# Performance work log

Measured on AMD Instinct MI355X. Metric: run time of the kernel, lower is better.

## Reference

```python
import jax, jax.numpy as jnp
from jax import lax
import numpy as np

WINDOW_SIZES = (1, 2, 3)


def _proj(x, w1, b1, w2, b2):
    # gated projection: sigmoid(Linear1) * tanh(Linear2)
    return jax.nn.sigmoid(x @ w1.T + b1) * jnp.tanh(x @ w2.T + b2)


def setup_inputs() -> dict:
    key = jax.random.key(0)
    ks = jax.random.split(key, 16)
    V, E, D = 50000, 1024, 1024
    N, La, Lq = 64, 512, 64
    s = 0.02  # weight scale to keep sigmoid/tanh unsaturated
    return {
        "data_q": jax.random.randint(ks[0], (Lq,), 0, V),
        "data_as": jax.random.randint(ks[1], (N, La), 0, V),
        "emb": jax.random.normal(ks[2], (V, E), jnp.float32),
        "w1": jax.random.normal(ks[3], (D, E), jnp.float32) * s,
        "b1": jnp.zeros((D,), jnp.float32),
        "w2": jax.random.normal(ks[4], (D, E), jnp.float32) * s,
        "b2": jnp.zeros((D,), jnp.float32),
        "cw1": jax.random.normal(ks[5], (D, D, 1), jnp.float32) * s,
        "cb1": jnp.zeros((D,), jnp.float32),
        "cw2": jax.random.normal(ks[6], (D, D, 2), jnp.float32) * s,
        "cb2": jnp.zeros((D,), jnp.float32),
        "cw3": jax.random.normal(ks[7], (D, D, 3), jnp.float32) * s,
        "cb3": jnp.zeros((D,), jnp.float32),
        "lin_w": jax.random.normal(ks[8], (D, 3 * D), jnp.float32) * s,
        "lin_b": jnp.zeros((D,), jnp.float32),
        "soft_w": jax.random.normal(ks[9], (1, D), jnp.float32) * s,
        "soft_b": jnp.zeros((1,), jnp.float32),
    }


def reference(data_q, data_as, emb, w1, b1, w2, b2,
              cw1, cb1, cw2, cb2, cw3, cb3, lin_w, lin_b, soft_w, soft_b):
    N, La = data_as.shape
    a_tok = data_as.reshape(-1)                     # [T] concatenated answers
    emb_a = emb[a_tok]                              # [T, E]
    emb_q = emb[data_q]                             # [Lq, E]
    pa = _proj(emb_a, w1, b1, w2, b2)               # [T, D]
    pq = _proj(emb_q, w1, b1, w2, b2)               # [Lq, D]

    # attention: M_r = q @ a^T ; alpha = softmax over question positions
    M = pq @ pa.T                                   # [Lq, T]
    alpha = jax.nn.softmax(M.T, axis=1)             # [T, Lq]
    Y = alpha @ pq                                  # [T, D]
    sim = pa * Y                                    # elementwise compare (mul)

    starts = jnp.arange(N) * La
    x = sim.T[None]                                 # [1, D, T]
    pools = []
    for w, cw, cb in zip(WINDOW_SIZES, (cw1, cw2, cw3), (cb1, cb2, cb3)):
        conv = lax.conv_general_dilated(
            x, cw, (1,), 'VALID',
            dimension_numbers=('NCW', 'OIW', 'NCW'))[0].T + cb  # [T-w+1, D]
        conv = jax.nn.relu(conv)
        # DMax: per-answer max over rows [start_k, start_k + La - w + 1)
        idx = starts[:, None] + jnp.arange(La - w + 1)[None, :]  # [N, La-w+1]
        pools.append(conv[idx].max(axis=1))          # [N, D]

    cat = jnp.concatenate(pools, axis=1)            # [N, 3D]
    h = jnp.tanh(cat @ lin_w.T + lin_b)             # [N, D]
    logits = (h @ soft_w.T + soft_b).reshape(-1)    # [N]
    return jax.nn.log_softmax(logits)
```

## Files before the change

kernel.cpp:

```cpp
#include <hip/hip_runtime.h>

#define DEV __device__ __forceinline__

typedef __bf16 bf16x8 __attribute__((ext_vector_type(8)));
typedef float f32x4 __attribute__((ext_vector_type(4)));
typedef unsigned short u16;
typedef u16 u16x4 __attribute__((ext_vector_type(4)));

constexpr int T_ANS = 32768;
constexpr int LQ    = 64;
constexpr int M_ALL = T_ANS + LQ;
constexpr int M_PAD = 32896;
constexpr int DIM   = 1024;

DEV u16 f2bf(float x) {
  unsigned u = __float_as_uint(x);
  return (u16)((u + 0x7FFFu + ((u >> 16) & 1u)) >> 16);
}
DEV float bf2f(u16 s) { return __uint_as_float(((unsigned)s) << 16); }

DEV void gl2lds16(const void* g, void* l) {
  __builtin_amdgcn_global_load_lds(
      (const __attribute__((address_space(1))) unsigned int*)g,
      (__attribute__((address_space(3))) unsigned int*)l, 16, 0, 0);
}


__global__ void cast4(const float* __restrict__ src, u16* __restrict__ dst, int n4) {
  int i = blockIdx.x * 256 + threadIdx.x;
  if (i < n4) {
    float4 v = ((const float4*)src)[i];
    u16x4 o = { f2bf(v.x), f2bf(v.y), f2bf(v.z), f2bf(v.w) };
    ((u16x4*)dst)[i] = o;
  }
}

template<int W>
__global__ void cast_conv_w(const float* __restrict__ src, u16* __restrict__ dst) {
  int i = blockIdx.x * 256 + threadIdx.x;
  if (i < 1024 * 1024) {
#pragma unroll
    for (int k = 0; k < W; ++k)
      dst[(size_t)k * (1024 * 1024) + i] = f2bf(src[(size_t)i * W + k]);
  }
}

__global__ void gather_cast(const int* __restrict__ dq, const int* __restrict__ das,
                            const float* __restrict__ emb, u16* __restrict__ X) {
  const int row = blockIdx.x;
  const int c   = threadIdx.x;
  size_t dsto = (size_t)row * DIM + c * 4;
  if (row >= M_ALL) {
    u16x4 z = {0, 0, 0, 0};
    *(u16x4*)(X + dsto) = z;
    return;
  }
  const int tok = (row < T_ANS) ? das[row] : dq[row - T_ANS];
  float4 v = ((const float4*)(emb + (size_t)tok * DIM))[c];
  u16x4 o = { f2bf(v.x), f2bf(v.y), f2bf(v.z), f2bf(v.w) };
  *(u16x4*)(X + dsto) = o;
}

__global__ void transpose_pq(const u16* __restrict__ pa, u16* __restrict__ pqT) {
  int i = blockIdx.x * 256 + threadIdx.x;
  int e = i >> 6, q = i & 63;
  pqT[i] = pa[(size_t)(T_ANS + q) * DIM + e];
}

__global__ void zero_pad_sim(u16* __restrict__ sim) {
  int i = blockIdx.x * 256 + threadIdx.x;
  if (i < 2 * DIM) sim[(size_t)T_ANS * DIM + i] = 0;
}

__global__ void cast_cat(const float* __restrict__ cat, u16* __restrict__ catb) {
  int i = blockIdx.x * 256 + threadIdx.x;
  if (i < 128 * 3072) {
    int row = i / 3072;
    catb[i] = (row < 64) ? f2bf(cat[i]) : (u16)0;
  }
}


__global__ __launch_bounds__(512, 2)
void proj_dual(const u16* __restrict__ X, const u16* __restrict__ B1,
               const u16* __restrict__ B2, const float* __restrict__ b1,
               const float* __restrict__ b2, u16* __restrict__ pa) {
  __shared__ alignas(16) u16 sA[128 * 32];
  __shared__ alignas(16) u16 sB1[128 * 32];
  __shared__ alignas(16) u16 sB2[128 * 32];
  const int tid = threadIdx.x, lane = tid & 63;
  const int tm = blockIdx.x * 128, tn = blockIdx.y * 128;
  const int wid = tid >> 6;
  const int wm = (wid >> 1) * 32, wn = (wid & 1) * 64;
  f32x4 acc1[2][4] = {}, acc2[2][4] = {};
  for (int k0 = 0; k0 < 1024; k0 += 32) {
    {
      const int f = tid * 16;
      const int r = f >> 6, cb = f & 63;
      gl2lds16((const char*)X  + (size_t)(tm + r) * 2048 + k0 * 2 + cb, (char*)sA  + f);
      gl2lds16((const char*)B1 + (size_t)(tn + r) * 2048 + k0 * 2 + cb, (char*)sB1 + f);
      gl2lds16((const char*)B2 + (size_t)(tn + r) * 2048 + k0 * 2 + cb, (char*)sB2 + f);
    }
    __syncthreads();
    const int lr = lane & 15, lk = (lane >> 4) * 8;
    bf16x8 af[2], bv1[4], bv2[4];
#pragma unroll
    for (int i = 0; i < 2; ++i)
      af[i]  = *(const bf16x8*)(sA  + (wm + i * 16 + lr) * 32 + lk);
#pragma unroll
    for (int i = 0; i < 4; ++i) {
      bv1[i] = *(const bf16x8*)(sB1 + (wn + i * 16 + lr) * 32 + lk);
      bv2[i] = *(const bf16x8*)(sB2 + (wn + i * 16 + lr) * 32 + lk);
    }
#pragma unroll
    for (int mi = 0; mi < 2; ++mi)
#pragma unroll
      for (int ni = 0; ni < 4; ++ni) {
        acc1[mi][ni] = __builtin_amdgcn_mfma_f32_16x16x32_bf16(af[mi], bv1[ni], acc1[mi][ni], 0, 0, 0);
        acc2[mi][ni] = __builtin_amdgcn_mfma_f32_16x16x32_bf16(af[mi], bv2[ni], acc2[mi][ni], 0, 0, 0);
      }
    __syncthreads();
  }
  const int lr = lane & 15, lg = (lane >> 4) * 4;
#pragma unroll
  for (int ni = 0; ni < 4; ++ni) {
    const int col = tn + wn + ni * 16 + lr;
    const float b1v = b1[col], b2v = b2[col];
#pragma unroll
    for (int mi = 0; mi < 2; ++mi)
#pragma unroll
      for (int r = 0; r < 4; ++r) {
        const int row = tm + wm + mi * 16 + lg + r;
        const float x1 = acc1[mi][ni][r] + b1v;
        const float x2 = acc2[mi][ni][r] + b2v;
        const float sg = 1.f / (1.f + __expf(-x1));
        const float th = 2.f / (1.f + __expf(-2.f * x2)) - 1.f;
        pa[(size_t)row * DIM + col] = f2bf(sg * th);
      }
  }
}


__global__ __launch_bounds__(256, 2)
void attn_s(const u16* __restrict__ pa, float* __restrict__ Spart) {
  __shared__ alignas(16) u16 sA[128 * 32];
  __shared__ alignas(16) u16 sB[64 * 32];
  const int tid = threadIdx.x, lane = tid & 63;
  const int tm = blockIdx.x * 128;
  const int kbase = blockIdx.y * 256;
  const int wid = tid >> 6;
  const int wm = (wid >> 1) * 64, wn = (wid & 1) * 32;
  const u16* pq = pa + (size_t)T_ANS * DIM;
  f32x4 acc[4][2] = {};
  for (int k0 = kbase; k0 < kbase + 256; k0 += 32) {
#pragma unroll
    for (int j = 0; j < 2; ++j) {
      const int f = tid * 16 + j * 4096;
      const int r = f >> 6, cb = f & 63;
      gl2lds16((const char*)pa + (size_t)(tm + r) * 2048 + k0 * 2 + cb, (char*)sA + f);
    }
    {
      const int f = tid * 16;
      const int r = f >> 6, cb = f & 63;
      gl2lds16((const char*)pq + (size_t)r * 2048 + k0 * 2 + cb, (char*)sB + f);
    }
    __syncthreads();
    const int lr = lane & 15, lk = (lane >> 4) * 8;
    bf16x8 af[4], bfr[2];
#pragma unroll
    for (int i = 0; i < 4; ++i)
      af[i] = *(const bf16x8*)(sA + (wm + i * 16 + lr) * 32 + lk);
#pragma unroll
    for (int i = 0; i < 2; ++i)
      bfr[i] = *(const bf16x8*)(sB + (wn + i * 16 + lr) * 32 + lk);
#pragma unroll
    for (int mi = 0; mi < 4; ++mi)
#pragma unroll
      for (int ni = 0; ni < 2; ++ni)
        acc[mi][ni] = __builtin_amdgcn_mfma_f32_16x16x32_bf16(af[mi], bfr[ni], acc[mi][ni], 0, 0, 0);
    __syncthreads();
  }
  const int lr = lane & 15, lg = (lane >> 4) * 4;
  float* Sp = Spart + (size_t)blockIdx.y * (T_ANS * 64);
#pragma unroll
  for (int mi = 0; mi < 4; ++mi)
#pragma unroll
    for (int ni = 0; ni < 2; ++ni)
#pragma unroll
      for (int r = 0; r < 4; ++r) {
        const int row = tm + wm + mi * 16 + lg + r;
        const int col = wn + ni * 16 + lr;
        Sp[(size_t)row * 64 + col] = acc[mi][ni][r];
      }
}

__global__ void softmax64(const float* __restrict__ Spart, u16* __restrict__ alpha) {
  const int row = blockIdx.x * 4 + (threadIdx.x >> 6);
  const int lane = threadIdx.x & 63;
  const size_t o = (size_t)row * 64 + lane;
  float v = Spart[o] + Spart[(size_t)1 * T_ANS * 64 + o]
          + Spart[(size_t)2 * T_ANS * 64 + o] + Spart[(size_t)3 * T_ANS * 64 + o];
  float m = v;
#pragma unroll
  for (int o2 = 32; o2 > 0; o2 >>= 1) m = fmaxf(m, __shfl_xor(m, o2));
  const float e = __expf(v - m);
  float s = e;
#pragma unroll
  for (int o2 = 32; o2 > 0; o2 >>= 1) s += __shfl_xor(s, o2);
  alpha[(size_t)row * 64 + lane] = f2bf(e / s);
}


__global__ __launch_bounds__(256, 2)
void attn_y_sim(const u16* __restrict__ alpha, const u16* __restrict__ pqT,
                const u16* __restrict__ pa, u16* __restrict__ sim) {
  __shared__ alignas(16) u16 sA[128 * 32];
  __shared__ alignas(16) u16 sB[128 * 32];
  const int tid = threadIdx.x, lane = tid & 63;
  const int tm = blockIdx.x * 128, tn = blockIdx.y * 128;
  const int wid = tid >> 6;
  const int wm = (wid >> 1) * 64, wn = (wid & 1) * 64;
  f32x4 acc[4][4] = {};
  for (int k0 = 0; k0 < 64; k0 += 32) {
#pragma unroll
    for (int j = 0; j < 2; ++j) {
      const int f = tid * 16 + j * 4096;
      const int r = f >> 6, cb = f & 63;
      gl2lds16((const char*)alpha + (size_t)(tm + r) * 128 + k0 * 2 + cb, (char*)sA + f);
      gl2lds16((const char*)pqT   + (size_t)(tn + r) * 128 + k0 * 2 + cb, (char*)sB + f);
    }
    __syncthreads();
    const int lr = lane & 15, lk = (lane >> 4) * 8;
    bf16x8 af[4], bfr[4];
#pragma unroll
    for (int i = 0; i < 4; ++i) {
      af[i]  = *(const bf16x8*)(sA + (wm + i * 16 + lr) * 32 + lk);
      bfr[i] = *(const bf16x8*)(sB + (wn + i * 16 + lr) * 32 + lk);
    }
#pragma unroll
    for (int mi = 0; mi < 4; ++mi)
#pragma unroll
      for (int ni = 0; ni < 4; ++ni)
        acc[mi][ni] = __builtin_amdgcn_mfma_f32_16x16x32_bf16(af[mi], bfr[ni], acc[mi][ni], 0, 0, 0);
    __syncthreads();
  }
  const int lr = lane & 15, lg = (lane >> 4) * 4;
#pragma unroll
  for (int ni = 0; ni < 4; ++ni) {
    const int col = tn + wn + ni * 16 + lr;
#pragma unroll
    for (int mi = 0; mi < 4; ++mi)
#pragma unroll
      for (int r = 0; r < 4; ++r) {
        const int row = tm + wm + mi * 16 + lg + r;
        const size_t o = (size_t)row * DIM + col;
        sim[o] = f2bf(bf2f(pa[o]) * acc[mi][ni][r]);
      }
  }
}


template<int W>
__global__ __launch_bounds__(256, 2)
void conv_pool(const u16* __restrict__ sim, const u16* __restrict__ Bw,
               const float* __restrict__ cb, float* __restrict__ cat) {
  __shared__ alignas(16) u16 sA[(128 + W) * 32];
  __shared__ alignas(16) u16 sB[W][128 * 32];
  const int tid = threadIdx.x, lane = tid & 63;
  const int tm = blockIdx.x * 128, tn = blockIdx.y * 128;
  const int wid = tid >> 6;
  const int wm = (wid >> 1) * 64, wn = (wid & 1) * 64;
  f32x4 acc[4][4] = {};
  for (int k0 = 0; k0 < 1024; k0 += 32) {
#pragma unroll
    for (int j = 0; j < 2; ++j) {
      const int f = tid * 16 + j * 4096;
      const int r = f >> 6, cbo = f & 63;
      gl2lds16((const char*)sim + (size_t)(tm + r) * 2048 + k0 * 2 + cbo, (char*)sA + f);
#pragma unroll
      for (int k = 0; k < W; ++k)
        gl2lds16((const char*)Bw + (size_t)k * 2097152 + (size_t)(tn + r) * 2048 + k0 * 2 + cbo,
                 (char*)&sB[k][0] + f);
    }
    if (W > 1 && tid < (W - 1) * 4) {
      const int f = 8192 + tid * 16;
      const int r = f >> 6, cbo = f & 63;
      gl2lds16((const char*)sim + (size_t)(tm + r) * 2048 + k0 * 2 + cbo, (char*)sA + f);
    }
    __syncthreads();
    const int lr = lane & 15, lk = (lane >> 4) * 8;
#pragma unroll
    for (int k = 0; k < W; ++k) {
      bf16x8 af[4], bfr[4];
#pragma unroll
      for (int i = 0; i < 4; ++i) {
        af[i]  = *(const bf16x8*)(sA + (wm + i * 16 + lr + k) * 32 + lk);
        bfr[i] = *(const bf16x8*)(&sB[k][0] + (wn + i * 16 + lr) * 32 + lk);
      }
#pragma unroll
      for (int mi = 0; mi < 4; ++mi)
#pragma unroll
        for (int ni = 0; ni < 4; ++ni)
          acc[mi][ni] = __builtin_amdgcn_mfma_f32_16x16x32_bf16(af[mi], bfr[ni], acc[mi][ni], 0, 0, 0);
    }
    __syncthreads();
  }
  const int lr = lane & 15, lg = (lane >> 4) * 4;
  const int n = tm >> 9;
#pragma unroll
  for (int ni = 0; ni < 4; ++ni) {
    const int col = tn + wn + ni * 16 + lr;
    const float cbv = cb[col];
    float vmax = 0.f;
#pragma unroll
    for (int mi = 0; mi < 4; ++mi)
#pragma unroll
      for (int r = 0; r < 4; ++r) {
        const int t = tm + wm + mi * 16 + lg + r;
        float v = fmaxf(acc[mi][ni][r] + cbv, 0.f);
        if ((t & 511) > 512 - W) v = 0.f;
        vmax = fmaxf(vmax, v);
      }
    vmax = fmaxf(vmax, __shfl_xor(vmax, 16));
    vmax = fmaxf(vmax, __shfl_xor(vmax, 32));
    if (lane < 16)
      atomicMax((int*)&cat[(size_t)n * 3072 + (W - 1) * 1024 + col], __float_as_int(vmax));
  }
}


__global__ __launch_bounds__(256, 2)
void final_h(const u16* __restrict__ catb, const u16* __restrict__ linb,
             const float* __restrict__ lin_b, float* __restrict__ h) {
  __shared__ alignas(16) u16 sA[128 * 32];
  __shared__ alignas(16) u16 sB[128 * 32];
  const int tid = threadIdx.x, lane = tid & 63;
  const int tn = blockIdx.y * 128;
  const int wid = tid >> 6;
  const int wm = (wid >> 1) * 64, wn = (wid & 1) * 64;
  f32x4 acc[4][4] = {};
  for (int k0 = 0; k0 < 3072; k0 += 32) {
#pragma unroll
    for (int j = 0; j < 2; ++j) {
      const int f = tid * 16 + j * 4096;
      const int r = f >> 6, cb = f & 63;
      gl2lds16((const char*)catb + (size_t)r * 6144 + k0 * 2 + cb, (char*)sA + f);
      gl2lds16((const char*)linb + (size_t)(tn + r) * 6144 + k0 * 2 + cb, (char*)sB + f);
    }
    __syncthreads();
    const int lr = lane & 15, lk = (lane >> 4) * 8;
    bf16x8 af[4], bfr[4];
#pragma unroll
    for (int i = 0; i < 4; ++i) {
      af[i]  = *(const bf16x8*)(sA + (wm + i * 16 + lr) * 32 + lk);
      bfr[i] = *(const bf16x8*)(sB + (wn + i * 16 + lr) * 32 + lk);
    }
#pragma unroll
    for (int mi = 0; mi < 4; ++mi)
#pragma unroll
      for (int ni = 0; ni < 4; ++ni)
        acc[mi][ni] = __builtin_amdgcn_mfma_f32_16x16x32_bf16(af[mi], bfr[ni], acc[mi][ni], 0, 0, 0);
    __syncthreads();
  }
  const int lr = lane & 15, lg = (lane >> 4) * 4;
#pragma unroll
  for (int ni = 0; ni < 4; ++ni) {
    const int col = tn + wn + ni * 16 + lr;
    const float bv = lin_b[col];
#pragma unroll
    for (int mi = 0; mi < 4; ++mi)
#pragma unroll
      for (int r = 0; r < 4; ++r) {
        const int row = wm + mi * 16 + lg + r;
        if (row < 64) {
          const float x = acc[mi][ni][r] + bv;
          h[(size_t)row * DIM + col] = 2.f / (1.f + __expf(-2.f * x)) - 1.f;
        }
      }
  }
}

__global__ void final_logits(const float* __restrict__ h, const float* __restrict__ soft_w,
                             const float* __restrict__ soft_b, float* __restrict__ out) {
  __shared__ float part[256];
  const int t = threadIdx.x;
  const int n = t >> 2, q = t & 3;
  float s = 0.f;
  for (int j = q * 256; j < q * 256 + 256; ++j) s += h[(size_t)n * DIM + j] * soft_w[j];
  part[t] = s;
  __syncthreads();
  if (t < 64) {
    float logit = part[t * 4] + part[t * 4 + 1] + part[t * 4 + 2] + part[t * 4 + 3] + soft_b[0];
    float m = logit;
#pragma unroll
    for (int o = 32; o > 0; o >>= 1) m = fmaxf(m, __shfl_xor(m, o));
    float e = __expf(logit - m);
    float ssum = e;
#pragma unroll
    for (int o = 32; o > 0; o >>= 1) ssum += __shfl_xor(ssum, o);
    out[t] = (logit - m) - logf(ssum);
  }
}


extern "C" void kernel_launch(void* const* d_in, const int* in_sizes, int n_in,
                              void* d_out, int out_size, void* d_ws, size_t ws_size,
                              hipStream_t stream) {
  const int*   data_q  = (const int*)d_in[0];
  const int*   data_as = (const int*)d_in[1];
  const float* emb     = (const float*)d_in[2];
  const float* w1      = (const float*)d_in[3];
  const float* b1      = (const float*)d_in[4];
  const float* w2      = (const float*)d_in[5];
  const float* b2      = (const float*)d_in[6];
  const float* cw1     = (const float*)d_in[7];
  const float* cb1     = (const float*)d_in[8];
  const float* cw2     = (const float*)d_in[9];
  const float* cb2     = (const float*)d_in[10];
  const float* cw3     = (const float*)d_in[11];
  const float* cb3     = (const float*)d_in[12];
  const float* lin_w   = (const float*)d_in[13];
  const float* lin_b   = (const float*)d_in[14];
  const float* soft_w  = (const float*)d_in[15];
  const float* soft_b  = (const float*)d_in[16];
  float* out = (float*)d_out;

  u16* X     = (u16*)d_ws;
  u16* pa    = X    + (size_t)M_PAD * DIM;
  u16* w1b   = pa   + (size_t)M_PAD * DIM;
  u16* w2b   = w1b  + 1024 * 1024;
  u16* cwb   = w2b  + 1024 * 1024;
  u16* linb  = cwb  + (size_t)6 * 1024 * 1024;
  u16* pqT   = linb + (size_t)3 * 1024 * 1024;
  u16* alpha = pqT  + 64 * 1024;
  float* Sold= (float*)(alpha + (size_t)T_ANS * 64);
  float* cat = Sold + (size_t)T_ANS * 64;
  u16* catb  = (u16*)(cat + 64 * 3072);
  float* h   = (float*)(catb + 128 * 3072);
  u16* simb  = X;
  float* Spart = (float*)X;

  hipMemsetAsync(cat, 0, 64 * 3072 * sizeof(float), stream);

  cast4<<<1024, 256, 0, stream>>>(w1, w1b, 1024 * 1024 / 4);
  cast4<<<1024, 256, 0, stream>>>(w2, w2b, 1024 * 1024 / 4);
  cast4<<<3072, 256, 0, stream>>>(lin_w, linb, 3072 * 1024 / 4);
  cast_conv_w<1><<<4096, 256, 0, stream>>>(cw1, cwb);
  cast_conv_w<2><<<4096, 256, 0, stream>>>(cw2, cwb + (size_t)1 * 1024 * 1024);
  cast_conv_w<3><<<4096, 256, 0, stream>>>(cw3, cwb + (size_t)3 * 1024 * 1024);

  gather_cast<<<M_PAD, 256, 0, stream>>>(data_q, data_as, emb, X);

  proj_dual<<<dim3(M_PAD / 128, 8), 512, 0, stream>>>(X, w1b, w2b, b1, b2, pa);
  transpose_pq<<<256, 256, 0, stream>>>(pa, pqT);

  attn_s<<<dim3(T_ANS / 128, 4), 256, 0, stream>>>(pa, Spart);
  softmax64<<<T_ANS / 4, 256, 0, stream>>>(Spart, alpha);
  attn_y_sim<<<dim3(T_ANS / 128, 8), 256, 0, stream>>>(alpha, pqT, pa, simb);
  zero_pad_sim<<<8, 256, 0, stream>>>(simb);

  conv_pool<1><<<dim3(T_ANS / 128, 8), 256, 0, stream>>>(simb, cwb, cb1, cat);
  conv_pool<2><<<dim3(T_ANS / 128, 8), 256, 0, stream>>>(simb, cwb + (size_t)1 * 1024 * 1024, cb2, cat);
  conv_pool<3><<<dim3(T_ANS / 128, 8), 256, 0, stream>>>(simb, cwb + (size_t)3 * 1024 * 1024, cb3, cat);

  cast_cat<<<1536, 256, 0, stream>>>(cat, catb);
  final_h<<<dim3(1, 8), 256, 0, stream>>>(catb, linb, lin_b, h);
  final_logits<<<1, 256, 0, stream>>>(h, soft_w, soft_b, out);
}
```

Baseline: 865.1 us.

## Replace projection and conv GEMMs with 256x256 double-buffered swizzled-LDS pipeline

Introduces a shared GEMM pipeline macro using 256x256 tiles, 128KB dynamic LDS, an XOR-swizzled layout, and double-buffered async global-to-LDS staging interleaved with MFMA phases under s_setprio and explicit waitcnt control. The projection now uses a single packed W12 weight that interleaves w1 and w2 in 16-row groups, so one GEMM yields both gates per tile. The conv kernels treat the W-tap convolution as a K=1024*W GEMM, with the shifted A rows addressed directly through the A pointer. M_PAD grows to fit 256-row tiles. The intent is to cut LDS traffic and exposed memory latency and raise MFMA utilisation, at the cost of one block per CU and fewer blocks in the grid.

Measured after the change: 930.7 us. 7.6% more time.

```diff
diff --git a/kernel.cpp b/kernel.cpp
--- a/kernel.cpp
+++ b/kernel.cpp
@@ -10,7 +10,7 @@
 constexpr int T_ANS = 32768;
 constexpr int LQ    = 64;
 constexpr int M_ALL = T_ANS + LQ;
-constexpr int M_PAD = 32896;
+constexpr int M_PAD = 33024;
 constexpr int DIM   = 1024;
 
 DEV u16 f2bf(float x) {
@@ -24,6 +24,93 @@
       (const __attribute__((address_space(1))) unsigned int*)g,
       (__attribute__((address_space(3))) unsigned int*)l, 16, 0, 0);
 }
+
+#define MF(A, B, C) __builtin_amdgcn_mfma_f32_16x16x32_bf16(A, B, C, 0, 0, 0)
+
+
+DEV void stageC(const char* gk, char* ldsT, int row0, int tid) {
+  const int f = tid << 4;
+  const int r = row0 + (f >> 7);
+  const int cb = ((f >> 4) & 7) ^ (r & 7);
+  gl2lds16(gk + (size_t)r * 2048 + (cb << 4), ldsT + (row0 << 7) + f);
+}
+
+DEV bf16x8 LF(const char* ldsT, int row, int cbyte) {
+  return *(const bf16x8*)(ldsT + (row << 7) + (cbyte ^ ((row & 7) << 4)));
+}
+
+#define PH(Q, LA, LB, STAGES, VMW)                                                     \
+  {                                                                                    \
+    bf16x8 a00 = LF(LA, wm + (2*(Q))*16 + lr, hi16);                                   \
+    bf16x8 a01 = LF(LA, wm + (2*(Q))*16 + lr, 64 + hi16);                              \
+    bf16x8 a10 = LF(LA, wm + (2*(Q)+1)*16 + lr, hi16);                                 \
+    bf16x8 a11 = LF(LA, wm + (2*(Q)+1)*16 + lr, 64 + hi16);                            \
+    bf16x8 b00 = LF(LB, wn +  0 + lr, hi16), b01 = LF(LB, wn +  0 + lr, 64 + hi16);    \
+    bf16x8 b10 = LF(LB, wn + 16 + lr, hi16), b11 = LF(LB, wn + 16 + lr, 64 + hi16);    \
+    bf16x8 b20 = LF(LB, wn + 32 + lr, hi16), b21 = LF(LB, wn + 32 + lr, 64 + hi16);    \
+    bf16x8 b30 = LF(LB, wn + 48 + lr, hi16), b31 = LF(LB, wn + 48 + lr, 64 + hi16);    \
+    STAGES                                                                             \
+    __builtin_amdgcn_s_barrier();                                                      \
+    asm volatile("s_waitcnt lgkmcnt(0)" ::: "memory");                                 \
+    __builtin_amdgcn_sched_barrier(0);                                                 \
+    __builtin_amdgcn_s_setprio(1);                                                     \
+    acc[2*(Q)][0] = MF(a00, b00, acc[2*(Q)][0]); acc[2*(Q)][0] = MF(a01, b01, acc[2*(Q)][0]); \
+    acc[2*(Q)][1] = MF(a00, b10, acc[2*(Q)][1]); acc[2*(Q)][1] = MF(a01, b11, acc[2*(Q)][1]); \
+    acc[2*(Q)][2] = MF(a00, b20, acc[2*(Q)][2]); acc[2*(Q)][2] = MF(a01, b21, acc[2*(Q)][2]); \
+    acc[2*(Q)][3] = MF(a00, b30, acc[2*(Q)][3]); acc[2*(Q)][3] = MF(a01, b31, acc[2*(Q)][3]); \
+    acc[2*(Q)+1][0] = MF(a10, b00, acc[2*(Q)+1][0]); acc[2*(Q)+1][0] = MF(a11, b01, acc[2*(Q)+1][0]); \
+    acc[2*(Q)+1][1] = MF(a10, b10, acc[2*(Q)+1][1]); acc[2*(Q)+1][1] = MF(a11, b11, acc[2*(Q)+1][1]); \
+    acc[2*(Q)+1][2] = MF(a10, b20, acc[2*(Q)+1][2]); acc[2*(Q)+1][2] = MF(a11, b21, acc[2*(Q)+1][2]); \
+    acc[2*(Q)+1][3] = MF(a10, b30, acc[2*(Q)+1][3]); acc[2*(Q)+1][3] = MF(a11, b31, acc[2*(Q)+1][3]); \
+    __builtin_amdgcn_s_setprio(0);                                                     \
+    VMW                                                                                \
+    __builtin_amdgcn_s_barrier();                                                      \
+  }
+
+#define VM2 asm volatile("s_waitcnt vmcnt(2)" ::: "memory"); __builtin_amdgcn_sched_barrier(0);
+#define VM0 asm volatile("s_waitcnt vmcnt(0)" ::: "memory"); __builtin_amdgcn_sched_barrier(0);
+
+#define GEMM_PIPE(KT)                                                                  \
+  const char* A0 = lds;            const char* B0c = lds + 32768;                      \
+  const char* A1 = lds + 65536;    const char* B1c = lds + 98304;                      \
+  char* A0w = lds; char* B0w = lds + 32768; char* A1w = lds + 65536; char* B1w = lds + 98304; \
+  f32x4 acc[8][4] = {};                                                                \
+                                              \
+  stageC(Ab(0), A0w, 0, tid);   stageC(Ab(0), A0w, 128, tid);                          \
+  stageC(Ab(0), A0w, 64, tid);  stageC(Ab(0), A0w, 192, tid);                          \
+  stageC(Bb(0), B0w, 0, tid);   stageC(Bb(0), B0w, 64, tid);                           \
+  stageC(Bb(0), B0w, 128, tid); stageC(Bb(0), B0w, 192, tid);                          \
+  stageC(Ab(1), A1w, 0, tid);   stageC(Ab(1), A1w, 128, tid);                          \
+  VM2                                                                                  \
+  __builtin_amdgcn_s_barrier();                                                        \
+  for (int i = 0; i < (KT)/2 - 1; ++i) {                                               \
+    const int kt1 = 2*i + 1;                                                           \
+    PH(0, A0, B0c,                                                                     \
+       stageC(Ab(kt1), A1w, 64, tid);  stageC(Ab(kt1), A1w, 192, tid);                 \
+       stageC(Bb(kt1), B1w, 0, tid);   stageC(Bb(kt1), B1w, 64, tid); , )              \
+    PH(1, A0, B0c, stageC(Bb(kt1), B1w, 128, tid); stageC(Bb(kt1), B1w, 192, tid); , ) \
+    PH(2, A0, B0c, stageC(Ab(kt1+1), A0w, 0, tid); stageC(Ab(kt1+1), A0w, 128, tid); , ) \
+    PH(3, A0, B0c, , VM2)                                                              \
+    PH(0, A1, B1c,                                                                     \
+       stageC(Ab(kt1+1), A0w, 64, tid); stageC(Ab(kt1+1), A0w, 192, tid);              \
+       stageC(Bb(kt1+1), B0w, 0, tid);  stageC(Bb(kt1+1), B0w, 64, tid); , )           \
+    PH(1, A1, B1c, stageC(Bb(kt1+1), B0w, 128, tid); stageC(Bb(kt1+1), B0w, 192, tid); , ) \
+    PH(2, A1, B1c, stageC(Ab(kt1+2), A1w, 0, tid); stageC(Ab(kt1+2), A1w, 128, tid); , ) \
+    PH(3, A1, B1c, , VM2)                                                              \
+  }                                                                                    \
+  {         \
+    const int kt1 = (KT) - 1;                                                          \
+    PH(0, A0, B0c,                                                                     \
+       stageC(Ab(kt1), A1w, 64, tid);  stageC(Ab(kt1), A1w, 192, tid);                 \
+       stageC(Bb(kt1), B1w, 0, tid);   stageC(Bb(kt1), B1w, 64, tid); , )              \
+    PH(1, A0, B0c, stageC(Bb(kt1), B1w, 128, tid); stageC(Bb(kt1), B1w, 192, tid); , ) \
+    PH(2, A0, B0c, , )                                                                 \
+    PH(3, A0, B0c, , VM0)                                                              \
+    PH(0, A1, B1c, , )                                                                 \
+    PH(1, A1, B1c, , )                                                                 \
+    PH(2, A1, B1c, , )                                                                 \
+    PH(3, A1, B1c, , )                                                                 \
+  }
 
 
 __global__ void cast4(const float* __restrict__ src, u16* __restrict__ dst, int n4) {
@@ -42,6 +129,17 @@
 #pragma unroll
     for (int k = 0; k < W; ++k)
       dst[(size_t)k * (1024 * 1024) + i] = f2bf(src[(size_t)i * W + k]);
+  }
+}
+
+__global__ void pack_w12(const float* __restrict__ w1, const float* __restrict__ w2,
+                         u16* __restrict__ W12) {
+  int i = blockIdx.x * 256 + threadIdx.x;
+  if (i < 2048 * 1024) {
+    int n2 = i >> 10, k = i & 1023;
+    int j = n2 >> 4, m = n2 & 15;
+    const float* src = (j & 1) ? w2 : w1;
+    W12[i] = f2bf(src[(size_t)((j >> 1) * 16 + m) * 1024 + k]);
   }
 }
 
@@ -81,62 +179,80 @@
 }
 
 
-__global__ __launch_bounds__(512, 2)
-void proj_dual(const u16* __restrict__ X, const u16* __restrict__ B1,
-               const u16* __restrict__ B2, const float* __restrict__ b1,
-               const float* __restrict__ b2, u16* __restrict__ pa) {
-  __shared__ alignas(16) u16 sA[128 * 32];
-  __shared__ alignas(16) u16 sB1[128 * 32];
-  __shared__ alignas(16) u16 sB2[128 * 32];
+__global__ __launch_bounds__(512, 1)
+void proj_g(const u16* __restrict__ X, const u16* __restrict__ W12,
+            const float* __restrict__ b1, const float* __restrict__ b2,
+            u16* __restrict__ pa) {
+  extern __shared__ char lds[];
   const int tid = threadIdx.x, lane = tid & 63;
-  const int tm = blockIdx.x * 128, tn = blockIdx.y * 128;
   const int wid = tid >> 6;
-  const int wm = (wid >> 1) * 32, wn = (wid & 1) * 64;
-  f32x4 acc1[2][4] = {}, acc2[2][4] = {};
-  for (int k0 = 0; k0 < 1024; k0 += 32) {
-    {
-      const int f = tid * 16;
-      const int r = f >> 6, cb = f & 63;
-      gl2lds16((const char*)X  + (size_t)(tm + r) * 2048 + k0 * 2 + cb, (char*)sA  + f);
-      gl2lds16((const char*)B1 + (size_t)(tn + r) * 2048 + k0 * 2 + cb, (char*)sB1 + f);
-      gl2lds16((const char*)B2 + (size_t)(tn + r) * 2048 + k0 * 2 + cb, (char*)sB2 + f);
-    }
-    __syncthreads();
-    const int lr = lane & 15, lk = (lane >> 4) * 8;
-    bf16x8 af[2], bv1[4], bv2[4];
-#pragma unroll
-    for (int i = 0; i < 2; ++i)
-      af[i]  = *(const bf16x8*)(sA  + (wm + i * 16 + lr) * 32 + lk);
-#pragma unroll
-    for (int i = 0; i < 4; ++i) {
-      bv1[i] = *(const bf16x8*)(sB1 + (wn + i * 16 + lr) * 32 + lk);
-      bv2[i] = *(const bf16x8*)(sB2 + (wn + i * 16 + lr) * 32 + lk);
-    }
-#pragma unroll
-    for (int mi = 0; mi < 2; ++mi)
-#pragma unroll
-      for (int ni = 0; ni < 4; ++ni) {
-        acc1[mi][ni] = __builtin_amdgcn_mfma_f32_16x16x32_bf16(af[mi], bv1[ni], acc1[mi][ni], 0, 0, 0);
-        acc2[mi][ni] = __builtin_amdgcn_mfma_f32_16x16x32_bf16(af[mi], bv2[ni], acc2[mi][ni], 0, 0, 0);
-      }
-    __syncthreads();
-  }
-  const int lr = lane & 15, lg = (lane >> 4) * 4;
-#pragma unroll
-  for (int ni = 0; ni < 4; ++ni) {
-    const int col = tn + wn + ni * 16 + lr;
+  const int wm = (wid >> 2) * 128, wn = (wid & 3) * 64;
+  const int lr = lane & 15, hi16 = (lane >> 4) * 16;
+  const int tm = blockIdx.x * 256, tn = blockIdx.y * 256;
+  const char* Ag = (const char*)X + (size_t)tm * 2048;
+  const char* Bg = (const char*)W12 + (size_t)tn * 2048;
+  auto Ab = [&](int kt) { return Ag + (kt >> 4) * 2048 + ((kt & 15) << 7); };
+  auto Bb = [&](int kt) { return Bg + (size_t)(kt >> 4) * 2097152 + ((kt & 15) << 7); };
+
+  GEMM_PIPE(16)
+
+  const int lg = (lane >> 4) * 4;
+#pragma unroll
+  for (int pp = 0; pp < 2; ++pp) {
+    const int col = (tn >> 1) + ((wn >> 5) + pp) * 16 + lr;
     const float b1v = b1[col], b2v = b2[col];
 #pragma unroll
-    for (int mi = 0; mi < 2; ++mi)
+    for (int mi = 0; mi < 8; ++mi)
 #pragma unroll
       for (int r = 0; r < 4; ++r) {
         const int row = tm + wm + mi * 16 + lg + r;
-        const float x1 = acc1[mi][ni][r] + b1v;
-        const float x2 = acc2[mi][ni][r] + b2v;
+        const float x1 = acc[mi][2 * pp][r] + b1v;
+        const float x2 = acc[mi][2 * pp + 1][r] + b2v;
         const float sg = 1.f / (1.f + __expf(-x1));
         const float th = 2.f / (1.f + __expf(-2.f * x2)) - 1.f;
         pa[(size_t)row * DIM + col] = f2bf(sg * th);
       }
+  }
+}
+
+
+template<int W>
+__global__ __launch_bounds__(512, 1)
+void conv_g(const u16* __restrict__ sim, const u16* __restrict__ Bw,
+            const float* __restrict__ cb, float* __restrict__ cat) {
+  extern __shared__ char lds[];
+  const int tid = threadIdx.x, lane = tid & 63;
+  const int wid = tid >> 6;
+  const int wm = (wid >> 2) * 128, wn = (wid & 3) * 64;
+  const int lr = lane & 15, hi16 = (lane >> 4) * 16;
+  const int tm = blockIdx.x * 256, tn = blockIdx.y * 256;
+  const char* Ag = (const char*)sim + (size_t)tm * 2048;
+  const char* Bg = (const char*)Bw + (size_t)tn * 2048;
+  auto Ab = [&](int kt) { return Ag + (kt >> 4) * 2048 + ((kt & 15) << 7); };
+  auto Bb = [&](int kt) { return Bg + (size_t)(kt >> 4) * 2097152 + ((kt & 15) << 7); };
+
+  GEMM_PIPE(16 * W)
+
+  const int lg = (lane >> 4) * 4;
+  const int n = tm >> 9;
+#pragma unroll
+  for (int ni = 0; ni < 4; ++ni) {
+    const int col = tn + wn + ni * 16 + lr;
+    const float cbv = cb[col];
+    float vmax = 0.f;
+#pragma unroll
+    for (int mi = 0; mi < 8; ++mi)
+#pragma unroll
+      for (int r = 0; r < 4; ++r) {
+        const int t = tm + wm + mi * 16 + lg + r;
+        float v = fmaxf(acc[mi][ni][r] + cbv, 0.f);
+        if ((t & 511) > 512 - W) v = 0.f;
+        vmax = fmaxf(vmax, v);
+      }
+    vmax = fmaxf(vmax, __shfl_xor(vmax, 16));
+    vmax = fmaxf(vmax, __shfl_xor(vmax, 32));
+    if (lane < 16)
+      atomicMax((int*)&cat[(size_t)n * 3072 + (W - 1) * 1024 + col], __float_as_int(vmax));
   }
 }
 
@@ -177,7 +293,7 @@
     for (int mi = 0; mi < 4; ++mi)
 #pragma unroll
       for (int ni = 0; ni < 2; ++ni)
-        acc[mi][ni] = __builtin_amdgcn_mfma_f32_16x16x32_bf16(af[mi], bfr[ni], acc[mi][ni], 0, 0, 0);
+        acc[mi][ni] = MF(af[mi], bfr[ni], acc[mi][ni]);
     __syncthreads();
   }
   const int lr = lane & 15, lg = (lane >> 4) * 4;
@@ -241,7 +357,7 @@
     for (int mi = 0; mi < 4; ++mi)
 #pragma unroll
       for (int ni = 0; ni < 4; ++ni)
-        acc[mi][ni] = __builtin_amdgcn_mfma_f32_16x16x32_bf16(af[mi], bfr[ni], acc[mi][ni], 0, 0, 0);
+        acc[mi][ni] = MF(af[mi], bfr[ni], acc[mi][ni]);
     __syncthreads();
   }
   const int lr = lane & 15, lg = (lane >> 4) * 4;
@@ -256,75 +372,6 @@
         const size_t o = (size_t)row * DIM + col;
         sim[o] = f2bf(bf2f(pa[o]) * acc[mi][ni][r]);
       }
-  }
-}
-
-
-template<int W>
-__global__ __launch_bounds__(256, 2)
-void conv_pool(const u16* __restrict__ sim, const u16* __restrict__ Bw,
-               const float* __restrict__ cb, float* __restrict__ cat) {
-  __shared__ alignas(16) u16 sA[(128 + W) * 32];
-  __shared__ alignas(16) u16 sB[W][128 * 32];
-  const int tid = threadIdx.x, lane = tid & 63;
-  const int tm = blockIdx.x * 128, tn = blockIdx.y * 128;
-  const int wid = tid >> 6;
-  const int wm = (wid >> 1) * 64, wn = (wid & 1) * 64;
-  f32x4 acc[4][4] = {};
-  for (int k0 = 0; k0 < 1024; k0 += 32) {
-#pragma unroll
-    for (int j = 0; j < 2; ++j) {
-      const int f = tid * 16 + j * 4096;
-      const int r = f >> 6, cbo = f & 63;
-      gl2lds16((const char*)sim + (size_t)(tm + r) * 2048 + k0 * 2 + cbo, (char*)sA + f);
-#pragma unroll
-      for (int k = 0; k < W; ++k)
-        gl2lds16((const char*)Bw + (size_t)k * 2097152 + (size_t)(tn + r) * 2048 + k0 * 2 + cbo,
-                 (char*)&sB[k][0] + f);
-    }
-    if (W > 1 && tid < (W - 1) * 4) {
-      const int f = 8192 + tid * 16;
-      const int r = f >> 6, cbo = f & 63;
-      gl2lds16((const char*)sim + (size_t)(tm + r) * 2048 + k0 * 2 + cbo, (char*)sA + f);
-    }
-    __syncthreads();
-    const int lr = lane & 15, lk = (lane >> 4) * 8;
-#pragma unroll
-    for (int k = 0; k < W; ++k) {
-      bf16x8 af[4], bfr[4];
-#pragma unroll
-      for (int i = 0; i < 4; ++i) {
-        af[i]  = *(const bf16x8*)(sA + (wm + i * 16 + lr + k) * 32 + lk);
-        bfr[i] = *(const bf16x8*)(&sB[k][0] + (wn + i * 16 + lr) * 32 + lk);
-      }
-#pragma unroll
-      for (int mi = 0; mi < 4; ++mi)
-#pragma unroll
-        for (int ni = 0; ni < 4; ++ni)
-          acc[mi][ni] = __builtin_amdgcn_mfma_f32_16x16x32_bf16(af[mi], bfr[ni], acc[mi][ni], 0, 0, 0);
-    }
-    __syncthreads();
-  }
-  const int lr = lane & 15, lg = (lane >> 4) * 4;
-  const int n = tm >> 9;
-#pragma unroll
-  for (int ni = 0; ni < 4; ++ni) {
-    const int col = tn + wn + ni * 16 + lr;
-    const float cbv = cb[col];
-    float vmax = 0.f;
-#pragma unroll
-    for (int mi = 0; mi < 4; ++mi)
-#pragma unroll
-      for (int r = 0; r < 4; ++r) {
-        const int t = tm + wm + mi * 16 + lg + r;
-        float v = fmaxf(acc[mi][ni][r] + cbv, 0.f);
-        if ((t & 511) > 512 - W) v = 0.f;
-        vmax = fmaxf(vmax, v);
-      }
-    vmax = fmaxf(vmax, __shfl_xor(vmax, 16));
-    vmax = fmaxf(vmax, __shfl_xor(vmax, 32));
-    if (lane < 16)
-      atomicMax((int*)&cat[(size_t)n * 3072 + (W - 1) * 1024 + col], __float_as_int(vmax));
   }
 }
 
@@ -359,7 +406,7 @@
     for (int mi = 0; mi < 4; ++mi)
 #pragma unroll
       for (int ni = 0; ni < 4; ++ni)
-        acc[mi][ni] = __builtin_amdgcn_mfma_f32_16x16x32_bf16(af[mi], bfr[ni], acc[mi][ni], 0, 0, 0);
+        acc[mi][ni] = MF(af[mi], bfr[ni], acc[mi][ni]);
     __syncthreads();
   }
   const int lr = lane & 15, lg = (lane >> 4) * 4;
@@ -425,16 +472,19 @@
   const float* soft_b  = (const float*)d_in[16];
   float* out = (float*)d_out;
 
+  hipFuncSetAttribute((const void*)proj_g, hipFuncAttributeMaxDynamicSharedMemorySize, 131072);
+  hipFuncSetAttribute((const void*)conv_g<1>, hipFuncAttributeMaxDynamicSharedMemorySize, 131072);
+  hipFuncSetAttribute((const void*)conv_g<2>, hipFuncAttributeMaxDynamicSharedMemorySize, 131072);
+  hipFuncSetAttribute((const void*)conv_g<3>, hipFuncAttributeMaxDynamicSharedMemorySize, 131072);
+
   u16* X     = (u16*)d_ws;
   u16* pa    = X    + (size_t)M_PAD * DIM;
-  u16* w1b   = pa   + (size_t)M_PAD * DIM;
-  u16* w2b   = w1b  + 1024 * 1024;
-  u16* cwb   = w2b  + 1024 * 1024;
+  u16* W12   = pa   + (size_t)M_PAD * DIM;
+  u16* cwb   = W12  + (size_t)2 * 1024 * 1024;
   u16* linb  = cwb  + (size_t)6 * 1024 * 1024;
   u16* pqT   = linb + (size_t)3 * 1024 * 1024;
   u16* alpha = pqT  + 64 * 1024;
-  float* Sold= (float*)(alpha + (size_t)T_ANS * 64);
-  float* cat = Sold + (size_t)T_ANS * 64;
+  float* cat = (float*)(alpha + (size_t)T_ANS * 64);
   u16* catb  = (u16*)(cat + 64 * 3072);
   float* h   = (float*)(catb + 128 * 3072);
   u16* simb  = X;
@@ -442,8 +492,7 @@
 
   hipMemsetAsync(cat, 0, 64 * 3072 * sizeof(float), stream);
 
-  cast4<<<1024, 256, 0, stream>>>(w1, w1b, 1024 * 1024 / 4);
-  cast4<<<1024, 256, 0, stream>>>(w2, w2b, 1024 * 1024 / 4);
+  pack_w12<<<8192, 256, 0, stream>>>(w1, w2, W12);
   cast4<<<3072, 256, 0, stream>>>(lin_w, linb, 3072 * 1024 / 4);
   cast_conv_w<1><<<4096, 256, 0, stream>>>(cw1, cwb);
   cast_conv_w<2><<<4096, 256, 0, stream>>>(cw2, cwb + (size_t)1 * 1024 * 1024);
@@ -451,7 +500,7 @@
 
   gather_cast<<<M_PAD, 256, 0, stream>>>(data_q, data_as, emb, X);
 
-  proj_dual<<<dim3(M_PAD / 128, 8), 512, 0, stream>>>(X, w1b, w2b, b1, b2, pa);
+  proj_g<<<dim3(M_PAD / 256, 8), 512, 131072, stream>>>(X, W12, b1, b2, pa);
   transpose_pq<<<256, 256, 0, stream>>>(pa, pqT);
 
   attn_s<<<dim3(T_ANS / 128, 4), 256, 0, stream>>>(pa, Spart);
@@ -459,9 +508,9 @@
   attn_y_sim<<<dim3(T_ANS / 128, 8), 256, 0, stream>>>(alpha, pqT, pa, simb);
   zero_pad_sim<<<8, 256, 0, stream>>>(simb);
 
-  conv_pool<1><<<dim3(T_ANS / 128, 8), 256, 0, stream>>>(simb, cwb, cb1, cat);
-  conv_pool<2><<<dim3(T_ANS / 128, 8), 256, 0, stream>>>(simb, cwb + (size_t)1 * 1024 * 1024, cb2, cat);
-  conv_pool<3><<<dim3(T_ANS / 128, 8), 256, 0, stream>>>(simb, cwb + (size_t)3 * 1024 * 1024, cb3, cat);
+  conv_g<1><<<dim3(T_ANS / 256, 4), 512, 131072, stream>>>(simb, cwb, cb1, cat);
+  conv_g<2><<<dim3(T_ANS / 256, 4), 512, 131072, stream>>>(simb, cwb + (size_t)1 * 1024 * 1024, cb2, cat);
+  conv_g<3><<<dim3(T_ANS / 256, 4), 512, 131072, stream>>>(simb, cwb + (size_t)3 * 1024 * 1024, cb3, cat);
 
   cast_cat<<<1536, 256, 0, stream>>>(cat, catb);
   final_h<<<dim3(1, 8), 256, 0, stream>>>(catb, linb, lin_b, h);
```
